# Kernel optimization log

Hardware: AMD Instinct MI355X
Metric: run time of the kernel (lower is better)

## Reference

```python
import jax, jax.numpy as jnp
import numpy as np

B, S, D = 4, 2048, 1024
H = 16
DH = D // H


def setup_inputs() -> dict:
    key = jax.random.key(0)
    ks = jax.random.split(key, 5)
    scale = 0.02
    return {
        "x": jax.random.normal(ks[0], (B, S, D), dtype=jnp.float32),
        "w_in": jax.random.normal(ks[1], (D, 3 * D), dtype=jnp.float32) * scale,
        "b_in": jax.random.normal(ks[2], (3 * D,), dtype=jnp.float32) * scale,
        "w_out": jax.random.normal(ks[3], (D, D), dtype=jnp.float32) * scale,
        "b_out": jax.random.normal(ks[4], (D,), dtype=jnp.float32) * scale,
        "causal_mask": 1,
    }


def reference(x, w_in, b_in, w_out, b_out, causal_mask):
    b, s, d = x.shape
    qkv = x @ w_in + b_in                       # [B,S,3D]
    q, k, v = jnp.split(qkv, 3, axis=-1)
    # [B,S,D] -> [B,H,S,DH]
    q = q.reshape(b, s, H, DH).transpose(0, 2, 1, 3)
    k = k.reshape(b, s, H, DH).transpose(0, 2, 1, 3)
    v = v.reshape(b, s, H, DH).transpose(0, 2, 1, 3)
    scores = jnp.einsum("bhqd,bhkd->bhqk", q, k)
    if causal_mask:
        # mask applied before scaling in original; -inf unaffected by scaling
        mask = jnp.triu(jnp.ones((s, s), dtype=bool), k=1)
        scores = jnp.where(mask, -jnp.inf, scores)
    scores = scores / jnp.sqrt(jnp.float32(DH))
    probs = jax.nn.softmax(scores, axis=-1)
    out = jnp.einsum("bhqk,bhkd->bhqd", probs, v)
    out = out.transpose(0, 2, 1, 3).reshape(b, s, d)
    return out @ w_out + b_out
```

## Files before the change

kernel.cpp:

```cpp
#include <hip/hip_runtime.h>
#include <hip/hip_bf16.h>
#include <cstdint>

#define NB 4
#define NS 2048
#define ND 1024
#define NH 16
#define NDH 64
#define NM (NB*NS)
#define N3D (3*ND)

typedef __attribute__((ext_vector_type(8))) short short8;
typedef __attribute__((ext_vector_type(4))) float f32x4;
typedef __attribute__((ext_vector_type(4))) unsigned short us4;
typedef __attribute__((ext_vector_type(4))) unsigned int uint4v;

__device__ __forceinline__ float bf2f(unsigned short u) {
  unsigned int i = ((unsigned int)u) << 16;
  return __builtin_bit_cast(float, i);
}
__device__ __forceinline__ unsigned short f2bf(float f) {
  unsigned int i = __builtin_bit_cast(unsigned int, f);
  i = (i + 0x7FFFu + ((i >> 16) & 1u)) >> 16;
  return (unsigned short)i;
}
__device__ __forceinline__ unsigned int cvtpk_bf16(float lo, float hi) {
  unsigned int r;
  asm("v_cvt_pk_bf16_f32 %0, %1, %2" : "=v"(r) : "v"(lo), "v"(hi));
  return r;
}

#define GLD16(g, l) __builtin_amdgcn_global_load_lds( \
    (__attribute__((address_space(1))) void*)(void*)(g), \
    (__attribute__((address_space(3))) void*)(l), 16, 0, 0)

__global__ __launch_bounds__(256) void cvt_bf16_k(
    const float* __restrict__ in, unsigned short* __restrict__ out, int n)
{
  const int i = (blockIdx.x * 256 + threadIdx.x) * 4;
  if (i + 3 < n) {
    const f32x4 v = *(const f32x4*)(in + i);
    us4 o = {f2bf(v[0]), f2bf(v[1]), f2bf(v[2]), f2bf(v[3])};
    *(us4*)(out + i) = o;
  }
}

__global__ __launch_bounds__(256) void transpose_cvt_k(
    const float* __restrict__ in, unsigned short* __restrict__ out,
    int rows, int cols)
{
  __shared__ unsigned short tile[32][33];
  const int c0 = blockIdx.x * 32, r0 = blockIdx.y * 32;
  const int tx = threadIdx.x & 31, ty = threadIdx.x >> 5;
  #pragma unroll
  for (int i = ty; i < 32; i += 8)
    tile[i][tx] = f2bf(in[(size_t)(r0 + i) * cols + (c0 + tx)]);
  __syncthreads();
  #pragma unroll
  for (int i = ty; i < 32; i += 8)
    out[(size_t)(c0 + i) * rows + (r0 + tx)] = tile[tx][i];
}

__global__ __launch_bounds__(256) void vt_transpose_k(
    const unsigned short* __restrict__ qkv, unsigned short* __restrict__ vt)
{
  __shared__ unsigned short tile[32][33];
  const int dt = blockIdx.x & 1;
  const int st = (blockIdx.x >> 1) & 63;
  const int bh = blockIdx.x >> 7;
  const int b = bh >> 4, h = bh & 15;
  const int tx = threadIdx.x & 31, ty = threadIdx.x >> 5;
  const int s0 = st * 32, d0 = dt * 32;
  const unsigned short* src = qkv + (size_t)b * NS * N3D + 2 * ND + h * NDH;
  #pragma unroll
  for (int i = ty; i < 32; i += 8)
    tile[i][tx] = src[(size_t)(s0 + i) * N3D + d0 + tx];
  __syncthreads();
  unsigned short* dst = vt + (size_t)bh * NDH * NS;
  #pragma unroll
  for (int i = ty; i < 32; i += 8)
    dst[(size_t)(d0 + i) * NS + s0 + tx] = tile[tx][i];
}

template<bool OUT_F32>
__global__ __launch_bounds__(256) void gemm_bt_bias(
    const unsigned short* __restrict__ A,
    const unsigned short* __restrict__ Bt,
    const float* __restrict__ bias,
    unsigned short* __restrict__ Cb,
    float* __restrict__ Cf,
    int M, int N, int K)
{
  __shared__ __align__(16) unsigned short Alds[2][128 * 64];
  __shared__ __align__(16) unsigned short Blds[2][128 * 64];
  const int nbn = N >> 7;
  const int nbm = M >> 7;
  const int xcd = blockIdx.x & 7;
  const int t   = blockIdx.x >> 3;
  const int bnpx = nbn >> 1;
  const int bn  = (xcd & 1) * bnpx + t % bnpx;
  const int bm  = (xcd >> 1) * (nbm >> 2) + t / bnpx;
  const int m0 = bm << 7, n0 = bn << 7;
  const int w = threadIdx.x >> 6, l = threadIdx.x & 63;
  const int wr = w >> 1, wc = w & 1;
  const int lr = l & 15, lg = l >> 4;

  const int sc = (l & 7) ^ (l >> 3);
  const unsigned short* gA = A + (size_t)(m0 + w * 32 + (l >> 3)) * K + sc * 8;
  const unsigned short* gB = Bt + (size_t)(n0 + w * 32 + (l >> 3)) * K + sc * 8;
  const int lwoff = (w * 32) * 64;

  auto stage = [&](int buf, int k0) {
    unsigned short* la = &Alds[buf][lwoff];
    unsigned short* lb = &Blds[buf][lwoff];
    #pragma unroll
    for (int r = 0; r < 4; ++r) {
      GLD16(gA + k0 + (size_t)(8 * r) * K, la + (8 * r) * 64);
      GLD16(gB + k0 + (size_t)(8 * r) * K, lb + (8 * r) * 64);
    }
  };

  f32x4 acc[4][4] = {};
  const int rxor = lr & 7;

  stage(0, 0);
  __syncthreads();

  #pragma unroll 1
  for (int it = 0; it < (K >> 6); ++it) {
    const int buf = it & 1;
    const int k0 = it << 6;
    if (k0 + 64 < K) stage(buf ^ 1, k0 + 64);

    #pragma unroll
    for (int kk = 0; kk < 2; ++kk) {
      const int rch = ((kk * 4 + lg) ^ rxor) << 3;
      short8 a[4], b[4];
      #pragma unroll
      for (int i = 0; i < 4; ++i)
        a[i] = *(const short8*)(&Alds[buf][(wr * 64 + i * 16 + lr) * 64 + rch]);
      #pragma unroll
      for (int j = 0; j < 4; ++j)
        b[j] = *(const short8*)(&Blds[buf][(wc * 64 + j * 16 + lr) * 64 + rch]);

      #pragma unroll
      for (int i = 0; i < 4; ++i)
        #pragma unroll
        for (int j = 0; j < 4; ++j)
          acc[i][j] = __builtin_amdgcn_mfma_f32_16x16x32_bf16(a[i], b[j], acc[i][j], 0, 0, 0);
    }

    __syncthreads();
  }

  #pragma unroll
  for (int j = 0; j < 4; ++j) {
    const int col = n0 + wc * 64 + j * 16 + lr;
    const float bv = bias[col];
    #pragma unroll
    for (int i = 0; i < 4; ++i) {
      #pragma unroll
      for (int r = 0; r < 4; ++r) {
        const int row = m0 + wr * 64 + i * 16 + lg * 4 + r;
        const float v = acc[i][j][r] + bv;
        if (OUT_F32) Cf[(size_t)row * N + col] = v;
        else         Cb[(size_t)row * N + col] = f2bf(v);
      }
    }
  }
}

__global__ __launch_bounds__(512) void attn_fwd(
    const unsigned short* __restrict__ qkv,
    const unsigned short* __restrict__ Vt,
    unsigned short* __restrict__ out)
{
  __shared__ __align__(16) char Kl[2][2][64 * 128];
  __shared__ __align__(16) char Vl[2][2][64 * 128];

  const int bid = blockIdx.x;
  const int bh = bid & 63;
  const int slot = bid >> 6;
  const int b = bh >> 4, h = bh & 15;
  const int w = threadIdx.x >> 6, l = threadIdx.x & 63;
  const int lr = l & 15, lg = l >> 4;

  const size_t rs = N3D;
  const unsigned short* Qb = qkv + (size_t)b * NS * rs + (size_t)h * NDH;
  const unsigned short* Kb = Qb + ND;
  const unsigned short* VtB = Vt + (size_t)bh * NDH * NS;

  const int srow = l >> 3;
  const int sw = (((l & 7) * 16) ^ (srow << 4)) >> 1;
  const unsigned short* KsrcBase = Kb + (size_t)(8 * w + srow) * rs + sw;
  const unsigned short* VsrcBase = VtB + (size_t)(8 * w + srow) * NS + sw;
  const int ldsRow0 = (8 * w) * 128;

  const float QSCALE = 0.125f * 1.44269504f;
  const int ksw = (lr & 7) << 4;

  #pragma unroll 1
  for (int pass = 0; pass < 2; ++pass) {
    const int qt = pass == 0 ? slot : 15 - slot;
    const int q0 = qt * 128 + w * 16;
    const int T2 = qt + 1;

    short8 qf[2];
    {
      const unsigned short* qrow = Qb + (size_t)(q0 + lr) * rs + lg * 8;
      qf[0] = *(const short8*)(qrow);
      qf[1] = *(const short8*)(qrow + 32);
      #pragma unroll
      for (int j = 0; j < 8; ++j) {
        qf[0][j] = (short)f2bf(bf2f((unsigned short)qf[0][j]) * QSCALE);
        qf[1][j] = (short)f2bf(bf2f((unsigned short)qf[1][j]) * QSCALE);
      }
    }

    float l_run = 0.f;
    f32x4 o[4] = {};

    auto stage = [&](int buf, int kt2) {
      const int kb = kt2 << 7;
      GLD16(KsrcBase + (size_t)kb * rs,        &Kl[buf][0][ldsRow0]);
      GLD16(KsrcBase + (size_t)(kb + 64) * rs, &Kl[buf][1][ldsRow0]);
      GLD16(VsrcBase + kb,                     &Vl[buf][0][ldsRow0]);
      GLD16(VsrcBase + kb + 64,                &Vl[buf][1][ldsRow0]);
    };

    stage(0, 0);
    __syncthreads();

    #pragma unroll 1
    for (int kt2 = 0; kt2 < T2; ++kt2) {
      const int cur = kt2 & 1;
      if (kt2 + 1 < T2) stage(cur ^ 1, kt2 + 1);

      #pragma unroll
      for (int st = 0; st < 2; ++st) {
        const int kbase = kt2 * 128 + st * 64;
        if (kbase > q0 + 15) continue;

        short8 kf[4][2];
        #pragma unroll
        for (int ks = 0; ks < 4; ++ks) {
          const char* rowp = &Kl[cur][st][(ks * 16 + lr) * 128];
          kf[ks][0] = *(const short8*)(rowp + ((lg * 16) ^ ksw));
          kf[ks][1] = *(const short8*)(rowp + ((64 + lg * 16) ^ ksw));
        }

        f32x4 s[4] = {};
        __builtin_amdgcn_s_setprio(1);
        #pragma unroll
        for (int ks = 0; ks < 4; ++ks) {
          s[ks] = __builtin_amdgcn_mfma_f32_16x16x32_bf16(kf[ks][0], qf[0], s[ks], 0, 0, 0);
          s[ks] = __builtin_amdgcn_mfma_f32_16x16x32_bf16(kf[ks][1], qf[1], s[ks], 0, 0, 0);
        }
        __builtin_amdgcn_s_setprio(0);

        short8 vf[4][2];
        #pragma unroll
        for (int nb = 0; nb < 4; ++nb) {
          const char* rowp = &Vl[cur][st][(nb * 16 + lr) * 128];
          vf[nb][0] = *(const short8*)(rowp + ((lg * 16) ^ ksw));
          vf[nb][1] = *(const short8*)(rowp + ((64 + lg * 16) ^ ksw));
        }

        const bool domask = (kbase + 63 > q0);
        const int qi = q0 + lr;
        float p[16];
        if (domask) {
          #pragma unroll
          for (int ks = 0; ks < 4; ++ks)
            #pragma unroll
            for (int r = 0; r < 4; ++r)
              p[ks * 4 + r] = (kbase + ks * 16 + lg * 4 + r > qi)
                                ? 0.f : exp2f(s[ks][r]);
        } else {
          #pragma unroll
          for (int ks = 0; ks < 4; ++ks)
            #pragma unroll
            for (int r = 0; r < 4; ++r)
              p[ks * 4 + r] = exp2f(s[ks][r]);
        }
        float s0 = (p[0] + p[1]) + (p[2] + p[3]);
        float s1 = (p[4] + p[5]) + (p[6] + p[7]);
        float s2 = (p[8] + p[9]) + (p[10] + p[11]);
        float s3 = (p[12] + p[13]) + (p[14] + p[15]);
        l_run += (s0 + s1) + (s2 + s3);

        unsigned A0 = cvtpk_bf16(p[0],  p[1]),  B0 = cvtpk_bf16(p[2],  p[3]);
        unsigned A1 = cvtpk_bf16(p[4],  p[5]),  B1 = cvtpk_bf16(p[6],  p[7]);
        unsigned A2 = cvtpk_bf16(p[8],  p[9]),  B2 = cvtpk_bf16(p[10], p[11]);
        unsigned A3 = cvtpk_bf16(p[12], p[13]), B3 = cvtpk_bf16(p[14], p[15]);

        asm("v_permlane32_swap_b32 %0, %1" : "+v"(A0), "+v"(A1));
        asm("v_permlane16_swap_b32 %0, %1" : "+v"(A0), "+v"(A1));
        asm("v_permlane32_swap_b32 %0, %1" : "+v"(B0), "+v"(B1));
        asm("v_permlane16_swap_b32 %0, %1" : "+v"(B0), "+v"(B1));
        asm("v_permlane32_swap_b32 %0, %1" : "+v"(A2), "+v"(A3));
        asm("v_permlane16_swap_b32 %0, %1" : "+v"(A2), "+v"(A3));
        asm("v_permlane32_swap_b32 %0, %1" : "+v"(B2), "+v"(B3));
        asm("v_permlane16_swap_b32 %0, %1" : "+v"(B2), "+v"(B3));

        uint4v u0 = {A0, B0, A1, B1};
        uint4v u1 = {A2, B2, A3, B3};
        short8 pf0 = __builtin_bit_cast(short8, u0);
        short8 pf1 = __builtin_bit_cast(short8, u1);

        __builtin_amdgcn_s_setprio(1);
        #pragma unroll
        for (int nb = 0; nb < 4; ++nb)
          o[nb] = __builtin_amdgcn_mfma_f32_16x16x32_bf16(pf0, vf[nb][0], o[nb], 0, 0, 0);
        #pragma unroll
        for (int nb = 0; nb < 4; ++nb)
          o[nb] = __builtin_amdgcn_mfma_f32_16x16x32_bf16(pf1, vf[nb][1], o[nb], 0, 0, 0);
        __builtin_amdgcn_s_setprio(0);
      }

      __syncthreads();
    }

    {
      float lt = l_run;
      lt += __shfl_xor(lt, 16);
      lt += __shfl_xor(lt, 32);
      #pragma unroll
      for (int rr = 0; rr < 4; ++rr) {
        const float lq = __shfl(lt, lg * 4 + rr);
        const float inv = 1.0f / lq;
        const int qi = q0 + lg * 4 + rr;
        #pragma unroll
        for (int nb = 0; nb < 4; ++nb)
          out[(size_t)(b * NS + qi) * ND + h * NDH + nb * 16 + lr] = f2bf(o[nb][rr] * inv);
      }
    }
  }
}

extern "C" void kernel_launch(void* const* d_in, const int* in_sizes, int n_in,
                              void* d_out, int out_size, void* d_ws, size_t ws_size,
                              hipStream_t stream) {
  const float* x     = (const float*)d_in[0];
  const float* w_in  = (const float*)d_in[1];
  const float* b_in  = (const float*)d_in[2];
  const float* w_out = (const float*)d_in[3];
  const float* b_out = (const float*)d_in[4];
  float* out = (float*)d_out;

  char* ws = (char*)d_ws;
  size_t off = 0;
  unsigned short* x_bf    = (unsigned short*)(ws + off); off += (size_t)NM * ND * 2;
  unsigned short* qkv     = (unsigned short*)(ws + off); off += (size_t)NM * N3D * 2;
  unsigned short* attn    = (unsigned short*)(ws + off); off += (size_t)NM * ND * 2;
  unsigned short* w_in_t  = (unsigned short*)(ws + off); off += (size_t)N3D * ND * 2;
  unsigned short* w_out_t = (unsigned short*)(ws + off); off += (size_t)ND * ND * 2;
  unsigned short* vt = x_bf;

  cvt_bf16_k<<<dim3((NM * ND) / (256 * 4)), 256, 0, stream>>>(x, x_bf, NM * ND);
  transpose_cvt_k<<<dim3(N3D / 32, ND / 32), 256, 0, stream>>>(w_in, w_in_t, ND, N3D);
  transpose_cvt_k<<<dim3(ND / 32, ND / 32), 256, 0, stream>>>(w_out, w_out_t, ND, ND);

  gemm_bt_bias<false><<<dim3((NM / 128) * (N3D / 128)), 256, 0, stream>>>(
      x_bf, w_in_t, b_in, qkv, nullptr, NM, N3D, ND);

  vt_transpose_k<<<dim3(64 * 64 * 2), 256, 0, stream>>>(qkv, vt);

  attn_fwd<<<dim3(64 * 8), 512, 0, stream>>>(qkv, vt, attn);

  gemm_bt_bias<true><<<dim3((NM / 128) * (ND / 128)), 256, 0, stream>>>(
      attn, w_out_t, b_out, nullptr, out, NM, ND, ND);
}
```

Baseline: 179.6 us.

## Retile GEMM to 128x256 with K-step 32 and fold Q scaling into QKV epilogue

```diff
diff --git a/kernel.cpp b/kernel.cpp
--- a/kernel.cpp
+++ b/kernel.cpp
@@ -33,6 +33,8 @@
 #define GLD16(g, l) __builtin_amdgcn_global_load_lds( \
     (__attribute__((address_space(1))) void*)(void*)(g), \
     (__attribute__((address_space(3))) void*)(l), 16, 0, 0)
+
+#define QSCALE_F (0.125f * 1.44269504f)
 
 __global__ __launch_bounds__(256) void cvt_bf16_k(
     const float* __restrict__ in, unsigned short* __restrict__ out, int n)
@@ -82,7 +84,7 @@
     dst[(size_t)(d0 + i) * NS + s0 + tx] = tile[tx][i];
 }
 
-template<bool OUT_F32>
+template<bool OUT_F32, bool SCALE_Q>
 __global__ __launch_bounds__(256) void gemm_bt_bias(
     const unsigned short* __restrict__ A,
     const unsigned short* __restrict__ Bt,
@@ -91,78 +93,74 @@
     float* __restrict__ Cf,
     int M, int N, int K)
 {
-  __shared__ __align__(16) unsigned short Alds[2][128 * 64];
-  __shared__ __align__(16) unsigned short Blds[2][128 * 64];
-  const int nbn = N >> 7;
+  __shared__ __align__(16) unsigned short Alds[2][128 * 32];
+  __shared__ __align__(16) unsigned short Blds[2][256 * 32];
+  const int nbn = N >> 8;
   const int nbm = M >> 7;
   const int xcd = blockIdx.x & 7;
   const int t   = blockIdx.x >> 3;
   const int bnpx = nbn >> 1;
   const int bn  = (xcd & 1) * bnpx + t % bnpx;
   const int bm  = (xcd >> 1) * (nbm >> 2) + t / bnpx;
-  const int m0 = bm << 7, n0 = bn << 7;
-  const int w = threadIdx.x >> 6, l = threadIdx.x & 63;
-  const int wr = w >> 1, wc = w & 1;
+  const int m0 = bm << 7, n0 = bn << 8;
+  const int tid = threadIdx.x;
+  const int w = tid >> 6, l = tid & 63;
   const int lr = l & 15, lg = l >> 4;
 
-  const int sc = (l & 7) ^ (l >> 3);
-  const unsigned short* gA = A + (size_t)(m0 + w * 32 + (l >> 3)) * K + sc * 8;
-  const unsigned short* gB = Bt + (size_t)(n0 + w * 32 + (l >> 3)) * K + sc * 8;
-  const int lwoff = (w * 32) * 64;
+  const int sc = (tid & 3) ^ ((tid >> 3) & 3);
+  const unsigned short* gA = A + (size_t)(m0 + (tid >> 2)) * K + sc * 8;
+  const unsigned short* gB = Bt + (size_t)(n0 + (tid >> 2)) * K + sc * 8;
+  const int lbase = 512 * w;
 
   auto stage = [&](int buf, int k0) {
-    unsigned short* la = &Alds[buf][lwoff];
-    unsigned short* lb = &Blds[buf][lwoff];
-    #pragma unroll
-    for (int r = 0; r < 4; ++r) {
-      GLD16(gA + k0 + (size_t)(8 * r) * K, la + (8 * r) * 64);
-      GLD16(gB + k0 + (size_t)(8 * r) * K, lb + (8 * r) * 64);
-    }
+    #pragma unroll
+    for (int i = 0; i < 2; ++i)
+      GLD16(gA + k0 + (size_t)(64 * i) * K, &Alds[buf][lbase + 2048 * i]);
+    #pragma unroll
+    for (int i = 0; i < 4; ++i)
+      GLD16(gB + k0 + (size_t)(64 * i) * K, &Blds[buf][lbase + 2048 * i]);
   };
 
-  f32x4 acc[4][4] = {};
-  const int rxor = lr & 7;
+  f32x4 acc[8][4] = {};
+  const int rch = ((lg ^ ((lr >> 1) & 3)) << 3);
 
   stage(0, 0);
   __syncthreads();
 
   #pragma unroll 1
-  for (int it = 0; it < (K >> 6); ++it) {
+  for (int it = 0; it < (K >> 5); ++it) {
     const int buf = it & 1;
-    const int k0 = it << 6;
-    if (k0 + 64 < K) stage(buf ^ 1, k0 + 64);
-
-    #pragma unroll
-    for (int kk = 0; kk < 2; ++kk) {
-      const int rch = ((kk * 4 + lg) ^ rxor) << 3;
-      short8 a[4], b[4];
-      #pragma unroll
-      for (int i = 0; i < 4; ++i)
-        a[i] = *(const short8*)(&Alds[buf][(wr * 64 + i * 16 + lr) * 64 + rch]);
+    const int k0 = it << 5;
+    if (k0 + 32 < K) stage(buf ^ 1, k0 + 32);
+
+    short8 a[8], b[4];
+    #pragma unroll
+    for (int i = 0; i < 8; ++i)
+      a[i] = *(const short8*)(&Alds[buf][(i * 16 + lr) * 32 + rch]);
+    #pragma unroll
+    for (int j = 0; j < 4; ++j)
+      b[j] = *(const short8*)(&Blds[buf][(w * 64 + j * 16 + lr) * 32 + rch]);
+
+    #pragma unroll
+    for (int i = 0; i < 8; ++i)
       #pragma unroll
       for (int j = 0; j < 4; ++j)
-        b[j] = *(const short8*)(&Blds[buf][(wc * 64 + j * 16 + lr) * 64 + rch]);
-
-      #pragma unroll
-      for (int i = 0; i < 4; ++i)
-        #pragma unroll
-        for (int j = 0; j < 4; ++j)
-          acc[i][j] = __builtin_amdgcn_mfma_f32_16x16x32_bf16(a[i], b[j], acc[i][j], 0, 0, 0);
-    }
+        acc[i][j] = __builtin_amdgcn_mfma_f32_16x16x32_bf16(a[i], b[j], acc[i][j], 0, 0, 0);
 
     __syncthreads();
   }
 
+  const float qs = (SCALE_Q && (n0 + w * 64) < ND) ? QSCALE_F : 1.0f;
   #pragma unroll
   for (int j = 0; j < 4; ++j) {
-    const int col = n0 + wc * 64 + j * 16 + lr;
+    const int col = n0 + w * 64 + j * 16 + lr;
     const float bv = bias[col];
     #pragma unroll
-    for (int i = 0; i < 4; ++i) {
+    for (int i = 0; i < 8; ++i) {
       #pragma unroll
       for (int r = 0; r < 4; ++r) {
-        const int row = m0 + wr * 64 + i * 16 + lg * 4 + r;
-        const float v = acc[i][j][r] + bv;
+        const int row = m0 + i * 16 + lg * 4 + r;
+        const float v = (acc[i][j][r] + bv) * qs;
         if (OUT_F32) Cf[(size_t)row * N + col] = v;
         else         Cb[(size_t)row * N + col] = f2bf(v);
       }
@@ -196,7 +194,6 @@
   const unsigned short* VsrcBase = VtB + (size_t)(8 * w + srow) * NS + sw;
   const int ldsRow0 = (8 * w) * 128;
 
-  const float QSCALE = 0.125f * 1.44269504f;
   const int ksw = (lr & 7) << 4;
 
   #pragma unroll 1
@@ -210,11 +207,6 @@
       const unsigned short* qrow = Qb + (size_t)(q0 + lr) * rs + lg * 8;
       qf[0] = *(const short8*)(qrow);
       qf[1] = *(const short8*)(qrow + 32);
-      #pragma unroll
-      for (int j = 0; j < 8; ++j) {
-        qf[0][j] = (short)f2bf(bf2f((unsigned short)qf[0][j]) * QSCALE);
-        qf[1][j] = (short)f2bf(bf2f((unsigned short)qf[1][j]) * QSCALE);
-      }
     }
 
     float l_run = 0.f;
@@ -361,13 +353,13 @@
   transpose_cvt_k<<<dim3(N3D / 32, ND / 32), 256, 0, stream>>>(w_in, w_in_t, ND, N3D);
   transpose_cvt_k<<<dim3(ND / 32, ND / 32), 256, 0, stream>>>(w_out, w_out_t, ND, ND);
 
-  gemm_bt_bias<false><<<dim3((NM / 128) * (N3D / 128)), 256, 0, stream>>>(
+  gemm_bt_bias<false, true><<<dim3((NM / 128) * (N3D / 256)), 256, 0, stream>>>(
       x_bf, w_in_t, b_in, qkv, nullptr, NM, N3D, ND);
 
   vt_transpose_k<<<dim3(64 * 64 * 2), 256, 0, stream>>>(qkv, vt);
 
   attn_fwd<<<dim3(64 * 8), 512, 0, stream>>>(qkv, vt, attn);
 
-  gemm_bt_bias<true><<<dim3((NM / 128) * (ND / 128)), 256, 0, stream>>>(
+  gemm_bt_bias<true, false><<<dim3((NM / 128) * (ND / 256)), 256, 0, stream>>>(
       attn, w_out_t, b_out, nullptr, out, NM, ND, ND);
 }
```

After: 236.9 us. +31.9%, slower.
